# Performance work log

Hardware: AMD Instinct MI355X
Metric: run time of the kernel (lower is better)

Reference implementation:

```python
import jax, jax.numpy as jnp
import numpy as np

DIM = 1024
HEADS = 8
HEAD_DIM = DIM // HEADS
D_STATE = 256
BATCH = 8192
DT_MIN = 1e-3
DT_MAX = 1e-1
EPS = 1e-4  # RMSNorm eps


def setup_inputs() -> dict:
    key = jax.random.key(0)
    ks = jax.random.split(key, 8)
    x_t = jax.random.normal(ks[0], (BATCH, DIM), dtype=jnp.float32)
    state_re = jax.random.normal(ks[1], (BATCH, HEADS, D_STATE), dtype=jnp.float32)
    state_im = jax.random.normal(ks[2], (BATCH, HEADS, D_STATE), dtype=jnp.float32)
    # parameters (match torch init)
    norm_weight = jnp.ones((DIM,), dtype=jnp.float32)
    A_re_log = jnp.full((HEADS, D_STATE), float(np.log(0.5)), dtype=jnp.float32)
    n = jnp.arange(1, D_STATE + 1, dtype=jnp.float32)
    A_im = jnp.broadcast_to(float(np.pi) * n, (HEADS, D_STATE)).astype(jnp.float32)
    b_scale = 1.0 / float(np.sqrt(HEAD_DIM))
    c_scale = 1.0 / float(np.sqrt(D_STATE))
    B_re = jax.random.normal(ks[3], (HEADS, D_STATE, HEAD_DIM), dtype=jnp.float32) * b_scale
    B_im = jax.random.normal(ks[4], (HEADS, D_STATE, HEAD_DIM), dtype=jnp.float32) * b_scale
    C_re = jax.random.normal(ks[5], (HEADS, HEAD_DIM, D_STATE), dtype=jnp.float32) * c_scale
    C_im = jax.random.normal(ks[6], (HEADS, HEAD_DIM, D_STATE), dtype=jnp.float32) * c_scale
    D = jnp.ones((DIM,), dtype=jnp.float32)
    # log_dt: inverse-softplus of log-uniform dt in [dt_min, dt_max]
    u = jax.random.uniform(ks[7], (HEADS, D_STATE), dtype=jnp.float32)
    dt = jnp.exp(u * (np.log(DT_MAX) - np.log(DT_MIN)) + np.log(DT_MIN))
    dt = jnp.maximum(dt, 1e-4)
    log_dt = dt + jnp.log(-jnp.expm1(-dt))
    return dict(x_t=x_t, state_re=state_re, state_im=state_im,
                norm_weight=norm_weight, A_re_log=A_re_log, A_im=A_im,
                B_re=B_re, B_im=B_im, C_re=C_re, C_im=C_im, D=D, log_dt=log_dt)


def reference(x_t, state_re, state_im, norm_weight, A_re_log, A_im,
              B_re, B_im, C_re, C_im, D, log_dt):
    batch = x_t.shape[0]
    # RMSNorm (eps=1e-4, elementwise affine)
    ms = jnp.mean(jnp.square(x_t), axis=-1, keepdims=True)
    x = x_t * jax.lax.rsqrt(ms + EPS) * norm_weight
    x_h = x.reshape(batch, HEADS, HEAD_DIM)  # (B,H,P)
    # discretize
    A = jax.lax.complex(-jnp.exp(A_re_log), A_im)            # (H,N)
    dt = jax.nn.softplus(log_dt)                              # (H,N)
    A_bar = jnp.exp(dt.astype(A.dtype) * A)                   # (H,N) complex
    B = jax.lax.complex(B_re, B_im)                           # (H,N,P)
    C = jax.lax.complex(C_re, C_im)                           # (H,P,N)
    B_bar = ((A_bar - 1.0) / A)[..., None] * B                # (H,N,P)
    # recurrent step
    state = jax.lax.complex(state_re, state_im)               # (B,H,N)
    Bx = jnp.einsum('hnp,bhp->bhn', B_bar, x_h.astype(B_bar.dtype))
    new_state = A_bar[None] * state + Bx                      # (B,H,N)
    Ch = jnp.einsum('hpn,bhn->bhp', C, new_state)             # (B,H,P)
    D_h = D.reshape(HEADS, HEAD_DIM)[None]                    # (1,H,P)
    y_h = 2.0 * Ch.real + D_h * x_h
    out = x_t + y_h.reshape(batch, DIM)
    return out, new_state.real, new_state.imag
```

## Files before the change

kernel.cpp:

```cpp
#include <hip/hip_runtime.h>

#define BATCH 8192
#define DIM 1024
#define HEADS 8
#define HEAD_DIM 128
#define DSTATE 256

typedef __attribute__((ext_vector_type(8))) short short8v;
typedef __attribute__((ext_vector_type(4))) float f32x4;
typedef __attribute__((ext_vector_type(4))) unsigned short ushort4v;
typedef __attribute__((ext_vector_type(4))) unsigned int uint4v;

__device__ __forceinline__ unsigned short f2bf(float x) {
  unsigned int u = __builtin_bit_cast(unsigned int, x);
  unsigned int r = u + 0x7FFFu + ((u >> 16) & 1u);
  return (unsigned short)(r >> 16);
}
__device__ __forceinline__ float bf2f(unsigned short h) {
  unsigned int u = ((unsigned int)h) << 16;
  return __builtin_bit_cast(float, u);
}

__device__ __forceinline__ void stage16f(const float* g, float* l) {
  __builtin_amdgcn_global_load_lds(
      (const __attribute__((address_space(1))) unsigned int*)g,
      (__attribute__((address_space(3))) unsigned int*)l, 16, 0, 0);
}
__device__ __forceinline__ void stage4u(const unsigned short* g, unsigned short* l) {
  __builtin_amdgcn_global_load_lds(
      (const __attribute__((address_space(1))) unsigned int*)g,
      (__attribute__((address_space(3))) unsigned int*)l, 4, 0, 0);
}

#define BARRIER() do { \
  asm volatile("s_waitcnt lgkmcnt(0)" ::: "memory"); \
  __builtin_amdgcn_s_barrier(); \
  asm volatile("" ::: "memory"); } while (0)


__global__ __launch_bounds__(256) void prep(
    const float* __restrict__ logdt, const float* __restrict__ arelog,
    const float* __restrict__ aim,
    const float* __restrict__ Bre, const float* __restrict__ Bim,
    const float* __restrict__ Cre, const float* __restrict__ Cim,
    const float* __restrict__ xtg, const float* __restrict__ normw,
    unsigned short* __restrict__ w1re, unsigned short* __restrict__ w1im,
    unsigned short* __restrict__ w2re, unsigned short* __restrict__ w2mi,
    float* __restrict__ abr, float* __restrict__ abi,
    float* __restrict__ scale, unsigned short* __restrict__ xtb) {
  const int blk = blockIdx.x;
  if (blk < 1024) {
    const int i = blk * 256 + threadIdx.x;
    const int p = i & 127, s = (i >> 7) & 255, h = i >> 15;
    const int kk = s >> 4, u = s & 15;
    const int n = ((kk >> 1) << 5) + ((u >> 2) & 3) * 8 + (kk & 1) * 4 + (u & 3);
    const int hn = h * 256 + n;
    const float ld = logdt[hn];
    const float dt = log1pf(expf(ld));
    const float Ar = -expf(arelog[hn]);
    const float Ai = aim[hn];
    const float e = expf(dt * Ar), th = dt * Ai;
    const float Abr = e * cosf(th), Abi = e * sinf(th);
    if (p == 0) { abr[h * 256 + s] = Abr; abi[h * 256 + s] = Abi; }
    const float den = Ar * Ar + Ai * Ai;
    const float br_ = Abr - 1.0f;
    const float cr = (br_ * Ar + Abi * Ai) / den;
    const float ci = (Abi * Ar - br_ * Ai) / den;
    const int src = hn * 128 + p;
    const float wb = normw[h * 128 + p];
    const float bre = Bre[src], bim = Bim[src];
    w1re[i] = f2bf((cr * bre - ci * bim) * wb);
    w1im[i] = f2bf((cr * bim + ci * bre) * wb);
  } else if (blk < 2048) {
    const int i = (blk - 1024) * 256 + threadIdx.x;
    w2re[i] = f2bf(Cre[i]);
    w2mi[i] = f2bf(-Cim[i]);
  } else {
    const int wid = threadIdx.x >> 6, lane = threadIdx.x & 63;
    const int row = (blk - 2048) * 4 + wid;
    const float* xr = xtg + (size_t)row * DIM;
    unsigned short* xo = xtb + (size_t)row * DIM;
    float ssq = 0.f;
    #pragma unroll
    for (int c = 0; c < 4; ++c) {
      const f32x4 v = *(const f32x4*)(xr + c * 256 + lane * 4);
      ssq += v[0]*v[0] + v[1]*v[1] + v[2]*v[2] + v[3]*v[3];
      ushort4v o;
      o[0] = f2bf(v[0]); o[1] = f2bf(v[1]); o[2] = f2bf(v[2]); o[3] = f2bf(v[3]);
      *(ushort4v*)(xo + c * 256 + lane * 4) = o;
    }
    #pragma unroll
    for (int m = 1; m < 64; m <<= 1) ssq += __shfl_xor(ssq, m, 64);
    if (lane == 0) scale[row] = rsqrtf(ssq * (1.0f / DIM) + 1e-4f);
  }
}

__global__ __launch_bounds__(512, 2) void s5_main(
    const unsigned short* __restrict__ w1re, const unsigned short* __restrict__ w1im,
    const unsigned short* __restrict__ w2re, const unsigned short* __restrict__ w2mi,
    const float* __restrict__ abrp, const float* __restrict__ abip,
    const float* __restrict__ scale, const unsigned short* __restrict__ xtb,
    const float* __restrict__ sre, const float* __restrict__ sim,
    const float* __restrict__ dvec, const float* __restrict__ normw,
    float* __restrict__ out, float* __restrict__ nsre, float* __restrict__ nsim) {
  __shared__ float Sb[3][2][16][256];
  __shared__ unsigned short xbL[3][16][128];
  __shared__ unsigned short pf[2][8][64][8];
  __shared__ float scL[256];
  const int tid = threadIdx.x;
  const int w = tid >> 6, lane = tid & 63;
  const int g = lane >> 4, bl = lane & 15;
  const int h = blockIdx.x & 7;
  const int blkrow = (blockIdx.x >> 3) * 256;

  short8v w1r[2][4], w1i[2][4];
  #pragma unroll
  for (int t = 0; t < 2; ++t) {
    const int kk = 2 * w + t;
    const unsigned short* pr = w1re + ((size_t)(h * DSTATE + kk * 16 + bl)) * HEAD_DIM + g * 8;
    const unsigned short* pi = w1im + ((size_t)(h * DSTATE + kk * 16 + bl)) * HEAD_DIM + g * 8;
    #pragma unroll
    for (int ks = 0; ks < 4; ++ks) {
      w1r[t][ks] = *(const short8v*)(pr + ks * 32);
      w1i[t][ks] = *(const short8v*)(pi + ks * 32);
    }
  }
  short8v w2r[8], w2i[8];
  {
    const unsigned short* qr = w2re + ((size_t)(h * HEAD_DIM + w * 16 + bl)) * DSTATE + g * 8;
    const unsigned short* qi = w2mi + ((size_t)(h * HEAD_DIM + w * 16 + bl)) * DSTATE + g * 8;
    #pragma unroll
    for (int j = 0; j < 8; ++j) {
      w2r[j] = *(const short8v*)(qr + j * 32);
      w2i[j] = *(const short8v*)(qi + j * 32);
    }
  }
  f32x4 Arh[2], Aih[2];
  #pragma unroll
  for (int t = 0; t < 2; ++t) {
    Arh[t] = *(const f32x4*)(abrp + h * DSTATE + (2 * w + t) * 16 + g * 4);
    Aih[t] = *(const f32x4*)(abip + h * DSTATE + (2 * w + t) * 16 + g * 4);
  }
  f32x4 d4;
  {
    const int col = h * HEAD_DIM + w * 16 + g * 4;
    const f32x4 dv = *(const f32x4*)(dvec + col);
    const f32x4 nv = *(const f32x4*)(normw + col);
    #pragma unroll
    for (int r = 0; r < 4; ++r) d4[r] = dv[r] * nv[r];
  }
  const int srcA = ((g >> 1) << 4) + bl;
  const int srcB = (((g >> 1) + 2) << 4) + bl;

  auto STAGE = [&](int t, int b) {
    const int gr0 = blkrow + t * 16;
    #pragma unroll
    for (int i = 0; i < 2; ++i) {
      const int row = 2 * w + i;
      const size_t rb = ((size_t)(gr0 + row) * HEADS + h) * DSTATE;
      const int soff = (lane ^ (row & 7)) * 4;
      stage16f(sre + rb + soff, &Sb[b][0][row][0]);
      stage16f(sim + rb + soff, &Sb[b][1][row][0]);
    }
    #pragma unroll
    for (int i = 0; i < 2; ++i) {
      const int row = 2 * w + i;
      const unsigned short* src = xtb + (size_t)(gr0 + row) * DIM + h * HEAD_DIM
          + (((lane >> 2) ^ (row & 7)) << 3) + ((lane & 3) << 1);
      stage4u(src, &xbL[b][row][0]);
    }
  };

  auto PHASE1 = [&](int t) {
    const int b = t % 3;
    const float scl = scL[t * 16 + bl];
    short8v xf[4];
    #pragma unroll
    for (int ks = 0; ks < 4; ++ks) {
      const int ch = (ks * 4 + g) ^ (bl & 7);
      uint4v u = *(const uint4v*)&xbL[b][bl][ch * 8];
      uint4v o;
      #pragma unroll
      for (int q = 0; q < 4; ++q) {
        const float lo = bf2f((unsigned short)(u[q] & 0xffffu)) * scl;
        const float hi = bf2f((unsigned short)(u[q] >> 16)) * scl;
        o[q] = (unsigned)f2bf(lo) | ((unsigned)f2bf(hi) << 16);
      }
      xf[ks] = __builtin_bit_cast(short8v, o);
    }
    f32x4 nre[2], nim[2];
    unsigned pr0 = 0, pr1 = 0, pi0 = 0, pi1 = 0;
    #pragma unroll
    for (int tt = 0; tt < 2; ++tt) {
      f32x4 dr = {0.f,0.f,0.f,0.f};
      f32x4 di = {0.f,0.f,0.f,0.f};
      #pragma unroll
      for (int ks = 0; ks < 4; ++ks)
        dr = __builtin_amdgcn_mfma_f32_16x16x32_bf16(w1r[tt][ks], xf[ks], dr, 0, 0, 0);
      #pragma unroll
      for (int ks = 0; ks < 4; ++ks)
        di = __builtin_amdgcn_mfma_f32_16x16x32_bf16(w1i[tt][ks], xf[ks], di, 0, 0, 0);
      const int c = (((8 * w + 2 * g + tt) ^ (bl & 7)) << 2);
      const f32x4 s_r = *(const f32x4*)&Sb[b][0][bl][c];
      const f32x4 s_i = *(const f32x4*)&Sb[b][1][bl][c];
      f32x4 nr, ni;
      #pragma unroll
      for (int r = 0; r < 4; ++r) {
        nr[r] = fmaf(Arh[tt][r], s_r[r], fmaf(-Aih[tt][r], s_i[r], dr[r]));
        ni[r] = fmaf(Arh[tt][r], s_i[r], fmaf(Aih[tt][r], s_r[r], di[r]));
      }
      nre[tt] = nr; nim[tt] = ni;
      unsigned lo  = (unsigned)f2bf(nr[0]) | ((unsigned)f2bf(nr[1]) << 16);
      unsigned hi  = (unsigned)f2bf(nr[2]) | ((unsigned)f2bf(nr[3]) << 16);
      unsigned lo2 = (unsigned)f2bf(ni[0]) | ((unsigned)f2bf(ni[1]) << 16);
      unsigned hi2 = (unsigned)f2bf(ni[2]) | ((unsigned)f2bf(ni[3]) << 16);
      if (tt == 0) { pr0 = lo; pr1 = hi; pi0 = lo2; pi1 = hi2; }
      else {
        uint4v urv; urv[0] = pr0; urv[1] = pr1; urv[2] = lo;  urv[3] = hi;
        uint4v uiv; uiv[0] = pi0; uiv[1] = pi1; uiv[2] = lo2; uiv[3] = hi2;
        *(short8v*)&pf[0][w][lane][0] = __builtin_bit_cast(short8v, urv);
        *(short8v*)&pf[1][w][lane][0] = __builtin_bit_cast(short8v, uiv);
      }
    }
    f32x4 v1r, v2r, v1i, v2i;
    #pragma unroll
    for (int e = 0; e < 4; ++e) {
      float a1 = __shfl(nre[0][e], srcA, 64);
      float b1 = __shfl(nre[1][e], srcA, 64);
      v1r[e] = (g & 1) ? b1 : a1;
      float a2 = __shfl(nre[0][e], srcB, 64);
      float b2 = __shfl(nre[1][e], srcB, 64);
      v2r[e] = (g & 1) ? b2 : a2;
      float c1 = __shfl(nim[0][e], srcA, 64);
      float d1 = __shfl(nim[1][e], srcA, 64);
      v1i[e] = (g & 1) ? d1 : c1;
      float c2 = __shfl(nim[0][e], srcB, 64);
      float d2 = __shfl(nim[1][e], srcB, 64);
      v2i[e] = (g & 1) ? d2 : c2;
    }
    const size_t no = ((size_t)(blkrow + t * 16 + bl) * HEADS + h) * DSTATE + w * 32 + g * 4;
    __builtin_nontemporal_store(v1r, (f32x4*)(nsre + no));
    __builtin_nontemporal_store(v2r, (f32x4*)(nsre + no + 16));
    __builtin_nontemporal_store(v1i, (f32x4*)(nsim + no));
    __builtin_nontemporal_store(v2i, (f32x4*)(nsim + no + 16));
  };

  auto PHASE2 = [&](int t) {
    const int b = t % 3;
    f32x4 a2 = {0.f,0.f,0.f,0.f};
    #pragma unroll
    for (int j = 0; j < 8; ++j) {
      const short8v pbr = *(const short8v*)&pf[0][j][lane][0];
      const short8v pbi = *(const short8v*)&pf[1][j][lane][0];
      a2 = __builtin_amdgcn_mfma_f32_16x16x32_bf16(w2r[j], pbr, a2, 0, 0, 0);
      a2 = __builtin_amdgcn_mfma_f32_16x16x32_bf16(w2i[j], pbi, a2, 0, 0, 0);
    }
    const float scl = scL[t * 16 + bl];
    const int col = h * HEAD_DIM + w * 16 + g * 4;
    const size_t o = (size_t)(blkrow + t * 16 + bl) * DIM + col;
    const unsigned short* xp =
        &xbL[b][bl][((((2 * w) + (g >> 1)) ^ (bl & 7)) << 3) + ((g & 1) << 2)];
    f32x4 ro;
    #pragma unroll
    for (int r = 0; r < 4; ++r) {
      const float xr = bf2f(xp[r]);
      ro[r] = xr * (1.0f + d4[r] * scl) + 2.0f * a2[r];
    }
    __builtin_nontemporal_store(ro, (f32x4*)(out + o));
  };

  if (w == 0) stage16f(scale + blkrow + lane * 4, &scL[0]);
  STAGE(0, 0);
  STAGE(1, 1);

  for (int t = 0; t < 16; ++t) {
    if (t == 0)      asm volatile("s_waitcnt vmcnt(6)"  ::: "memory");
    else if (t == 1) asm volatile("s_waitcnt vmcnt(11)" ::: "memory");
    else if (t <= 14) asm volatile("s_waitcnt vmcnt(16)" ::: "memory");
    else             asm volatile("s_waitcnt vmcnt(10)" ::: "memory");
    BARRIER();
    if (t + 2 < 16) STAGE(t + 2, (t + 2) % 3);
    __builtin_amdgcn_sched_barrier(0);
    PHASE1(t);
    BARRIER();
    PHASE2(t);
  }
}

extern "C" void kernel_launch(void* const* d_in, const int* in_sizes, int n_in,
                              void* d_out, int out_size, void* d_ws, size_t ws_size,
                              hipStream_t stream) {
  const float* x_t      = (const float*)d_in[0];
  const float* state_re = (const float*)d_in[1];
  const float* state_im = (const float*)d_in[2];
  const float* norm_w   = (const float*)d_in[3];
  const float* A_re_log = (const float*)d_in[4];
  const float* A_im     = (const float*)d_in[5];
  const float* B_re     = (const float*)d_in[6];
  const float* B_im     = (const float*)d_in[7];
  const float* C_re     = (const float*)d_in[8];
  const float* C_im     = (const float*)d_in[9];
  const float* Dv       = (const float*)d_in[10];
  const float* log_dt   = (const float*)d_in[11];

  float* out   = (float*)d_out;
  float* ns_re = out + (size_t)BATCH * DIM;
  float* ns_im = ns_re + (size_t)BATCH * HEADS * DSTATE;

  char* ws = (char*)d_ws;
  unsigned short* w1re = (unsigned short*)ws;
  unsigned short* w1im = w1re + 262144;
  unsigned short* w2re = w1im + 262144;
  unsigned short* w2mi = w2re + 262144;
  float* abr   = (float*)(ws + 4 * 524288);
  float* abi   = abr + 2048;
  float* scale = abi + 2048;
  unsigned short* xtb = (unsigned short*)(scale + 8192);

  prep<<<4096, 256, 0, stream>>>(log_dt, A_re_log, A_im, B_re, B_im, C_re, C_im,
                                 x_t, norm_w, w1re, w1im, w2re, w2mi,
                                 abr, abi, scale, xtb);
  s5_main<<<256, 512, 0, stream>>>(w1re, w1im, w2re, w2mi, abr, abi, scale, xtb,
                                   state_re, state_im, Dv, norm_w,
                                   out, ns_re, ns_im);
}
```

Measured before the change: 91.15 us.

## Software-pipeline phase 2 one tile behind phase 1 and drop mid-loop barrier

Double-buffers the phase-1 to phase-2 LDS exchange buffer and grows the x staging ring to four slots. This lets phase 2 of tile t-1 run in the same barrier interval as phase 1 of tile t, removing one block barrier per iteration and letting the second GEMM overlap the first. The vmcnt waits are retuned for the new schedule. The output and state stores also change from nontemporal to regular stores, which alters cache behaviour for the write stream. The extra LDS may affect occupancy at 2 blocks per CU.

Result: slower. 97.38 us (+6.8%).

```diff
diff --git a/kernel.cpp b/kernel.cpp
--- a/kernel.cpp
+++ b/kernel.cpp
@@ -104,8 +104,8 @@
     const float* __restrict__ dvec, const float* __restrict__ normw,
     float* __restrict__ out, float* __restrict__ nsre, float* __restrict__ nsim) {
   __shared__ float Sb[3][2][16][256];
-  __shared__ unsigned short xbL[3][16][128];
-  __shared__ unsigned short pf[2][8][64][8];
+  __shared__ unsigned short xbL[4][16][128];
+  __shared__ unsigned short pf[2][2][8][64][8];
   __shared__ float scL[256];
   const int tid = threadIdx.x;
   const int w = tid >> 6, lane = tid & 63;
@@ -152,33 +152,34 @@
   const int srcA = ((g >> 1) << 4) + bl;
   const int srcB = (((g >> 1) + 2) << 4) + bl;
 
-  auto STAGE = [&](int t, int b) {
+  auto STAGE = [&](int t) {
+    const int b3 = t % 3, b4 = t & 3;
     const int gr0 = blkrow + t * 16;
     #pragma unroll
     for (int i = 0; i < 2; ++i) {
       const int row = 2 * w + i;
       const size_t rb = ((size_t)(gr0 + row) * HEADS + h) * DSTATE;
       const int soff = (lane ^ (row & 7)) * 4;
-      stage16f(sre + rb + soff, &Sb[b][0][row][0]);
-      stage16f(sim + rb + soff, &Sb[b][1][row][0]);
+      stage16f(sre + rb + soff, &Sb[b3][0][row][0]);
+      stage16f(sim + rb + soff, &Sb[b3][1][row][0]);
     }
     #pragma unroll
     for (int i = 0; i < 2; ++i) {
       const int row = 2 * w + i;
       const unsigned short* src = xtb + (size_t)(gr0 + row) * DIM + h * HEAD_DIM
           + (((lane >> 2) ^ (row & 7)) << 3) + ((lane & 3) << 1);
-      stage4u(src, &xbL[b][row][0]);
+      stage4u(src, &xbL[b4][row][0]);
     }
   };
 
   auto PHASE1 = [&](int t) {
-    const int b = t % 3;
+    const int b3 = t % 3, b4 = t & 3, pb = t & 1;
     const float scl = scL[t * 16 + bl];
     short8v xf[4];
     #pragma unroll
     for (int ks = 0; ks < 4; ++ks) {
       const int ch = (ks * 4 + g) ^ (bl & 7);
-      uint4v u = *(const uint4v*)&xbL[b][bl][ch * 8];
+      uint4v u = *(const uint4v*)&xbL[b4][bl][ch * 8];
       uint4v o;
       #pragma unroll
       for (int q = 0; q < 4; ++q) {
@@ -201,8 +202,8 @@
       for (int ks = 0; ks < 4; ++ks)
         di = __builtin_amdgcn_mfma_f32_16x16x32_bf16(w1i[tt][ks], xf[ks], di, 0, 0, 0);
       const int c = (((8 * w + 2 * g + tt) ^ (bl & 7)) << 2);
-      const f32x4 s_r = *(const f32x4*)&Sb[b][0][bl][c];
-      const f32x4 s_i = *(const f32x4*)&Sb[b][1][bl][c];
+      const f32x4 s_r = *(const f32x4*)&Sb[b3][0][bl][c];
+      const f32x4 s_i = *(const f32x4*)&Sb[b3][1][bl][c];
       f32x4 nr, ni;
       #pragma unroll
       for (int r = 0; r < 4; ++r) {
@@ -218,8 +219,8 @@
       else {
         uint4v urv; urv[0] = pr0; urv[1] = pr1; urv[2] = lo;  urv[3] = hi;
         uint4v uiv; uiv[0] = pi0; uiv[1] = pi1; uiv[2] = lo2; uiv[3] = hi2;
-        *(short8v*)&pf[0][w][lane][0] = __builtin_bit_cast(short8v, urv);
-        *(short8v*)&pf[1][w][lane][0] = __builtin_bit_cast(short8v, uiv);
+        *(short8v*)&pf[pb][0][w][lane][0] = __builtin_bit_cast(short8v, urv);
+        *(short8v*)&pf[pb][1][w][lane][0] = __builtin_bit_cast(short8v, uiv);
       }
     }
     f32x4 v1r, v2r, v1i, v2i;
@@ -239,19 +240,19 @@
       v2i[e] = (g & 1) ? d2 : c2;
     }
     const size_t no = ((size_t)(blkrow + t * 16 + bl) * HEADS + h) * DSTATE + w * 32 + g * 4;
-    __builtin_nontemporal_store(v1r, (f32x4*)(nsre + no));
-    __builtin_nontemporal_store(v2r, (f32x4*)(nsre + no + 16));
-    __builtin_nontemporal_store(v1i, (f32x4*)(nsim + no));
-    __builtin_nontemporal_store(v2i, (f32x4*)(nsim + no + 16));
+    *(f32x4*)(nsre + no)      = v1r;
+    *(f32x4*)(nsre + no + 16) = v2r;
+    *(f32x4*)(nsim + no)      = v1i;
+    *(f32x4*)(nsim + no + 16) = v2i;
   };
 
   auto PHASE2 = [&](int t) {
-    const int b = t % 3;
+    const int b4 = t & 3, pb = t & 1;
     f32x4 a2 = {0.f,0.f,0.f,0.f};
     #pragma unroll
     for (int j = 0; j < 8; ++j) {
-      const short8v pbr = *(const short8v*)&pf[0][j][lane][0];
-      const short8v pbi = *(const short8v*)&pf[1][j][lane][0];
+      const short8v pbr = *(const short8v*)&pf[pb][0][j][lane][0];
+      const short8v pbi = *(const short8v*)&pf[pb][1][j][lane][0];
       a2 = __builtin_amdgcn_mfma_f32_16x16x32_bf16(w2r[j], pbr, a2, 0, 0, 0);
       a2 = __builtin_amdgcn_mfma_f32_16x16x32_bf16(w2i[j], pbi, a2, 0, 0, 0);
     }
@@ -259,32 +260,34 @@
     const int col = h * HEAD_DIM + w * 16 + g * 4;
     const size_t o = (size_t)(blkrow + t * 16 + bl) * DIM + col;
     const unsigned short* xp =
-        &xbL[b][bl][((((2 * w) + (g >> 1)) ^ (bl & 7)) << 3) + ((g & 1) << 2)];
+        &xbL[b4][bl][((((2 * w) + (g >> 1)) ^ (bl & 7)) << 3) + ((g & 1) << 2)];
     f32x4 ro;
     #pragma unroll
     for (int r = 0; r < 4; ++r) {
       const float xr = bf2f(xp[r]);
       ro[r] = xr * (1.0f + d4[r] * scl) + 2.0f * a2[r];
     }
-    __builtin_nontemporal_store(ro, (f32x4*)(out + o));
+    *(f32x4*)(out + o) = ro;
   };
 
   if (w == 0) stage16f(scale + blkrow + lane * 4, &scL[0]);
-  STAGE(0, 0);
-  STAGE(1, 1);
+  STAGE(0);
+  STAGE(1);
 
   for (int t = 0; t < 16; ++t) {
-    if (t == 0)      asm volatile("s_waitcnt vmcnt(6)"  ::: "memory");
-    else if (t == 1) asm volatile("s_waitcnt vmcnt(11)" ::: "memory");
+    if (t == 0)       asm volatile("s_waitcnt vmcnt(6)"  ::: "memory");
+    else if (t == 1)  asm volatile("s_waitcnt vmcnt(10)" ::: "memory");
+    else if (t == 2)  asm volatile("s_waitcnt vmcnt(15)" ::: "memory");
     else if (t <= 14) asm volatile("s_waitcnt vmcnt(16)" ::: "memory");
-    else             asm volatile("s_waitcnt vmcnt(10)" ::: "memory");
+    else              asm volatile("s_waitcnt vmcnt(10)" ::: "memory");
     BARRIER();
-    if (t + 2 < 16) STAGE(t + 2, (t + 2) % 3);
+    if (t + 2 < 16) STAGE(t + 2);
     __builtin_amdgcn_sched_barrier(0);
+    if (t > 0) PHASE2(t - 1);
     PHASE1(t);
-    BARRIER();
-    PHASE2(t);
-  }
+  }
+  BARRIER();
+  PHASE2(15);
 }
 
 extern "C" void kernel_launch(void* const* d_in, const int* in_sizes, int n_in,
```
